# Performance work log

Measured on AMD Instinct MI355X. Metric: run time of the kernel, lower is better.

## Reference

```python
import jax, jax.numpy as jnp
import numpy as np

INPUT_DIM = 1024
OUT_DIM = 1024
ORDER = 4
EXPANSION_POINT = 0.0


def setup_inputs() -> dict:
    key = jax.random.key(0)
    k_x, k_c = jax.random.split(key)
    x = jax.random.normal(k_x, (8192, INPUT_DIM), dtype=jnp.float32)
    coeffs = jax.random.normal(k_c, (OUT_DIM, INPUT_DIM, ORDER), dtype=jnp.float32) * 0.01
    bias = jnp.zeros((1, OUT_DIM), dtype=jnp.float32)
    return {"x": x, "coeffs": coeffs, "bias": bias}


def reference(x, coeffs, bias):
    # x: [..., input_dim] -> flatten leading dims
    outshape = x.shape[:-1] + (OUT_DIM,)
    xf = x.reshape(-1, INPUT_DIM)
    x_shifted = xf - EXPANSION_POINT
    # powers P[n, i, k] = x_shifted^k, k = 0..order-1 (0**0 == 1, matching torch)
    powers = jnp.power(x_shifted[:, :, None], jnp.arange(ORDER, dtype=x.dtype))
    # y[n, o] = sum_{i,k} P[n,i,k] * coeffs[o,i,k]  -- single GEMM-like contraction
    y = jnp.einsum('nik,oik->no', powers, coeffs)
    y = y + bias
    return y.reshape(outshape)
```

## Files before the change

kernel.cpp:

```cpp
#include <hip/hip_runtime.h>
#include <stdint.h>

#define IN_DIM 1024
#define OUT_DIM 1024
#define NROWS 8192
#define KD 3072

#define BM 256
#define BN 128
#define BK 64
#define NT (KD / BK)

typedef __bf16 bf16x8 __attribute__((ext_vector_type(8)));
typedef float f32x4 __attribute__((ext_vector_type(4)));
typedef unsigned short us8 __attribute__((ext_vector_type(8)));
typedef unsigned int u32;

#define AS1 __attribute__((address_space(1)))
#define AS3 __attribute__((address_space(3)))

__device__ __forceinline__ unsigned short f2bf(float f) {
    u32 u = __builtin_bit_cast(u32, f);
    u32 r = (u + 0x7fffu + ((u >> 16) & 1u)) >> 16;
    return (unsigned short)r;
}

__global__ __launch_bounds__(256) void prep_coeffs(const float* __restrict__ c,
                                                   const float* __restrict__ bias,
                                                   unsigned short* __restrict__ B,
                                                   float* __restrict__ bias2) {
    const int o = blockIdx.x;
    const float4* row = reinterpret_cast<const float4*>(c + (size_t)o * (IN_DIM * 4));
    unsigned short* Bo = B + (size_t)o * KD;
    float s = 0.f;
    for (int i = threadIdx.x; i < IN_DIM; i += 256) {
        float4 v = row[i];
        s += v.x;
        Bo[i]        = f2bf(v.y);
        Bo[1024 + i] = f2bf(v.z);
        Bo[2048 + i] = f2bf(v.w);
    }
#pragma unroll
    for (int off = 32; off; off >>= 1) s += __shfl_down(s, off);
    __shared__ float red[4];
    if ((threadIdx.x & 63) == 0) red[threadIdx.x >> 6] = s;
    __syncthreads();
    if (threadIdx.x == 0) bias2[o] = bias[o] + red[0] + red[1] + red[2] + red[3];
}

__global__ __launch_bounds__(256) void prep_powers(const float* __restrict__ x,
                                                   unsigned short* __restrict__ A) {
    int t = blockIdx.x * blockDim.x + threadIdx.x;
    int n = t >> 8;
    int i4 = (t & 255) * 4;
    float4 v = reinterpret_cast<const float4*>(x)[t];
    unsigned short* An = A + (size_t)n * KD + i4;
    float xs[4] = {v.x, v.y, v.z, v.w};
    unsigned short b1[4], b2[4], b3[4];
#pragma unroll
    for (int j = 0; j < 4; ++j) {
        float x1 = xs[j], x2 = x1 * x1, x3 = x2 * x1;
        b1[j] = f2bf(x1); b2[j] = f2bf(x2); b3[j] = f2bf(x3);
    }
    ushort4 p1 = {b1[0], b1[1], b1[2], b1[3]};
    ushort4 p2 = {b2[0], b2[1], b2[2], b2[3]};
    ushort4 p3 = {b3[0], b3[1], b3[2], b3[3]};
    *reinterpret_cast<ushort4*>(An)        = p1;
    *reinterpret_cast<ushort4*>(An + 1024) = p2;
    *reinterpret_cast<ushort4*>(An + 2048) = p3;
}

__global__ __launch_bounds__(512, 1) void taylor_gemm(
    const unsigned short* __restrict__ A,
    const unsigned short* __restrict__ B,
    const float* __restrict__ bias2,
    float* __restrict__ C) {
    __shared__ alignas(16) unsigned short sA[3][BM * BK];
    __shared__ alignas(16) unsigned short sB[3][BN * BK];

    const int tid = threadIdx.x;
    const int lane = tid & 63;
    const int wid = tid >> 6;
    const int wr = wid >> 1;
    const int wc = wid & 1;
    const int gx = blockIdx.x, gy = blockIdx.y;

    const char* Ab = (const char*)A;
    const char* Bb = (const char*)B;
    const int cs = ((lane & 7) ^ (lane >> 3)) * 8;
    size_t aSrc[4], bSrc[2];
    int aDst[4], bDst[2];
#pragma unroll
    for (int u = 0; u < 4; ++u) {
        int row = gx * BM + u * 64 + wid * 8 + (lane >> 3);
        aSrc[u] = ((size_t)row * KD + cs) * 2;
        aDst[u] = (u * 64 + wid * 8) * BK;
    }
#pragma unroll
    for (int u = 0; u < 2; ++u) {
        int row = gy * BN + u * 64 + wid * 8 + (lane >> 3);
        bSrc[u] = ((size_t)row * KD + cs) * 2;
        bDst[u] = (u * 64 + wid * 8) * BK;
    }

    auto stage_unit = [&](int b, int kt, int u) {
        size_t koff = (size_t)kt * (BK * 2);
        if (u < 4)
            __builtin_amdgcn_global_load_lds(
                (const AS1 void*)(Ab + aSrc[u] + koff),
                (AS3 void*)(&sA[b][aDst[u]]), 16, 0, 0);
        else
            __builtin_amdgcn_global_load_lds(
                (const AS1 void*)(Bb + bSrc[u - 4] + koff),
                (AS3 void*)(&sB[b][bDst[u - 4]]), 16, 0, 0);
    };

    int aSw[2], bSw[2];
#pragma unroll
    for (int ks = 0; ks < 2; ++ks) {
        int sw = ((ks * 4 + (lane >> 4)) ^ (lane & 7)) * 8;
        aSw[ks] = (wr * 64 + (lane & 15)) * BK + sw;
        bSw[ks] = (wc * 64 + (lane & 15)) * BK + sw;
    }

    f32x4 acc[4][4] = {};

#pragma unroll
    for (int u = 0; u < 6; ++u) stage_unit(0, 0, u);
#pragma unroll
    for (int u = 0; u < 6; ++u) stage_unit(1, 1, u);

    for (int kt = 0; kt < NT; ++kt) {
        const int cb = kt % 3;
        const int nb = (kt + 2) % 3;
        if (kt < NT - 1) asm volatile("s_waitcnt vmcnt(6)" ::: "memory");
        else             asm volatile("s_waitcnt vmcnt(0)" ::: "memory");
        __builtin_amdgcn_s_barrier();
        __builtin_amdgcn_sched_barrier(0);

        const unsigned short* sAc = &sA[cb][0];
        const unsigned short* sBc = &sB[cb][0];
        const bool doStage = (kt < NT - 2);

        bf16x8 bfr[4][2];
#pragma unroll
        for (int n = 0; n < 4; ++n)
#pragma unroll
            for (int ks = 0; ks < 2; ++ks)
                bfr[n][ks] = __builtin_bit_cast(bf16x8,
                    *reinterpret_cast<const us8*>(&sBc[bSw[ks] + n * 16 * BK]));

#pragma unroll
        for (int m = 0; m < 4; ++m) {
            bf16x8 af[2];
#pragma unroll
            for (int ks = 0; ks < 2; ++ks)
                af[ks] = __builtin_bit_cast(bf16x8,
                    *reinterpret_cast<const us8*>(&sAc[aSw[ks] + m * 16 * BK]));
            if (doStage) {
                stage_unit(nb, kt + 2, m);
                if (m < 2) stage_unit(nb, kt + 2, 4 + m);
            }
            asm volatile("s_waitcnt lgkmcnt(0)" ::: "memory");
            __builtin_amdgcn_sched_barrier(0);
            __builtin_amdgcn_s_setprio(1);
#pragma unroll
            for (int n = 0; n < 4; ++n)
#pragma unroll
                for (int ks = 0; ks < 2; ++ks)
                    acc[m][n] = __builtin_amdgcn_mfma_f32_16x16x32_bf16(
                        af[ks], bfr[n][ks], acc[m][n], 0, 0, 0);
            __builtin_amdgcn_s_setprio(0);
        }
    }

    const int colBase = gy * BN + wc * 64 + (lane & 15);
    const int rowBase = gx * BM + wr * 64 + (lane >> 4) * 4;
#pragma unroll
    for (int n = 0; n < 4; ++n) {
        int col = colBase + n * 16;
        float bv = bias2[col];
#pragma unroll
        for (int m = 0; m < 4; ++m) {
            int row = rowBase + m * 16;
#pragma unroll
            for (int r = 0; r < 4; ++r)
                C[(size_t)(row + r) * OUT_DIM + col] = acc[m][n][r] + bv;
        }
    }
}

__global__ void taylor_naive(const float* __restrict__ x, const float* __restrict__ coeffs,
                             const float* __restrict__ bias, float* __restrict__ out) {
    int n = blockIdx.x;
    __shared__ float P[IN_DIM * 4];
    for (int i = threadIdx.x; i < IN_DIM; i += blockDim.x) {
        float xv = x[(size_t)n * IN_DIM + i];
        P[i * 4 + 0] = 1.f;
        P[i * 4 + 1] = xv;
        P[i * 4 + 2] = xv * xv;
        P[i * 4 + 3] = xv * xv * xv;
    }
    __syncthreads();
    for (int o = threadIdx.x; o < OUT_DIM; o += blockDim.x) {
        float s = bias[o];
        const float* c = coeffs + (size_t)o * (IN_DIM * 4);
        for (int i = 0; i < IN_DIM; ++i) {
            float4 cv = *reinterpret_cast<const float4*>(c + i * 4);
            s += cv.x * P[i * 4 + 0] + cv.y * P[i * 4 + 1] +
                 cv.z * P[i * 4 + 2] + cv.w * P[i * 4 + 3];
        }
        out[(size_t)n * OUT_DIM + o] = s;
    }
}

extern "C" void kernel_launch(void* const* d_in, const int* in_sizes, int n_in,
                              void* d_out, int out_size, void* d_ws, size_t ws_size,
                              hipStream_t stream) {
    const float* x = (const float*)d_in[0];
    const float* coeffs = (const float*)d_in[1];
    const float* bias = (const float*)d_in[2];
    float* out = (float*)d_out;

    const size_t needA = (size_t)NROWS * KD * 2;
    const size_t needB = (size_t)OUT_DIM * KD * 2;
    const size_t needBias = OUT_DIM * sizeof(float);

    if (ws_size >= needA + needB + needBias) {
        unsigned short* A = (unsigned short*)d_ws;
        unsigned short* B = (unsigned short*)((char*)d_ws + needA);
        float* bias2 = (float*)((char*)d_ws + needA + needB);
        prep_coeffs<<<OUT_DIM, 256, 0, stream>>>(coeffs, bias, B, bias2);
        prep_powers<<<(NROWS * IN_DIM / 4) / 256, 256, 0, stream>>>(x, A);
        dim3 grid(NROWS / BM, OUT_DIM / BN);
        taylor_gemm<<<grid, 512, 0, stream>>>(A, B, bias2, out);
    } else {
        taylor_naive<<<NROWS, 256, 0, stream>>>(x, coeffs, bias, out);
    }
}
```

Measured before the change: 90.06 us.

## Double-buffer LDS fragments in registers and overlap reads with MFMA

Restructures the GEMM main loop so the next k-tile's LDS fragments are loaded into a second register set while the current tile's 32 MFMAs run, unrolled by two to ping-pong register buffers. Global-to-LDS staging is now issued all at once per iteration, with a full vmcnt(0) wait. Launch bounds are raised to two blocks per CU. Together these aim to hide LDS latency and raise occupancy, at the cost of roughly doubled fragment registers, which could spill under the tighter register budget. The full vmcnt wait may also expose global load latency, and the LDS footprint may not actually allow two blocks per CU.

```diff
diff --git a/kernel.cpp b/kernel.cpp
--- a/kernel.cpp
+++ b/kernel.cpp
@@ -23,6 +23,10 @@
     u32 u = __builtin_bit_cast(u32, f);
     u32 r = (u + 0x7fffu + ((u >> 16) & 1u)) >> 16;
     return (unsigned short)r;
+}
+
+__device__ __forceinline__ bf16x8 ld8(const unsigned short* p) {
+    return __builtin_bit_cast(bf16x8, *reinterpret_cast<const us8*>(p));
 }
 
 __global__ __launch_bounds__(256) void prep_coeffs(const float* __restrict__ c,
@@ -70,7 +74,7 @@
     *reinterpret_cast<ushort4*>(An + 2048) = p3;
 }
 
-__global__ __launch_bounds__(512, 1) void taylor_gemm(
+__global__ __launch_bounds__(512, 2) void taylor_gemm(
     const unsigned short* __restrict__ A,
     const unsigned short* __restrict__ B,
     const float* __restrict__ bias2,
@@ -103,16 +107,18 @@
         bDst[u] = (u * 64 + wid * 8) * BK;
     }
 
-    auto stage_unit = [&](int b, int kt, int u) {
+    auto stage_all = [&](int b, int kt) {
         size_t koff = (size_t)kt * (BK * 2);
-        if (u < 4)
+#pragma unroll
+        for (int u = 0; u < 4; ++u)
             __builtin_amdgcn_global_load_lds(
                 (const AS1 void*)(Ab + aSrc[u] + koff),
                 (AS3 void*)(&sA[b][aDst[u]]), 16, 0, 0);
-        else
+#pragma unroll
+        for (int u = 0; u < 2; ++u)
             __builtin_amdgcn_global_load_lds(
-                (const AS1 void*)(Bb + bSrc[u - 4] + koff),
-                (AS3 void*)(&sB[b][bDst[u - 4]]), 16, 0, 0);
+                (const AS1 void*)(Bb + bSrc[u] + koff),
+                (AS3 void*)(&sB[b][bDst[u]]), 16, 0, 0);
     };
 
     int aSw[2], bSw[2];
@@ -123,56 +129,60 @@
         bSw[ks] = (wc * 64 + (lane & 15)) * BK + sw;
     }
 
+    bf16x8 fa0[4][2], fb0[4][2], fa1[4][2], fb1[4][2];
     f32x4 acc[4][4] = {};
 
-#pragma unroll
-    for (int u = 0; u < 6; ++u) stage_unit(0, 0, u);
-#pragma unroll
-    for (int u = 0; u < 6; ++u) stage_unit(1, 1, u);
-
-    for (int kt = 0; kt < NT; ++kt) {
-        const int cb = kt % 3;
-        const int nb = (kt + 2) % 3;
-        if (kt < NT - 1) asm volatile("s_waitcnt vmcnt(6)" ::: "memory");
-        else             asm volatile("s_waitcnt vmcnt(0)" ::: "memory");
-        __builtin_amdgcn_s_barrier();
-        __builtin_amdgcn_sched_barrier(0);
-
-        const unsigned short* sAc = &sA[cb][0];
-        const unsigned short* sBc = &sB[cb][0];
-        const bool doStage = (kt < NT - 2);
-
-        bf16x8 bfr[4][2];
+    auto read_frags = [&](bf16x8 (&fa)[4][2], bf16x8 (&fb)[4][2], int b) {
+        const unsigned short* sAc = &sA[b][0];
+        const unsigned short* sBc = &sB[b][0];
 #pragma unroll
         for (int n = 0; n < 4; ++n)
 #pragma unroll
             for (int ks = 0; ks < 2; ++ks)
-                bfr[n][ks] = __builtin_bit_cast(bf16x8,
-                    *reinterpret_cast<const us8*>(&sBc[bSw[ks] + n * 16 * BK]));
-
-#pragma unroll
-        for (int m = 0; m < 4; ++m) {
-            bf16x8 af[2];
+                fb[n][ks] = ld8(&sBc[bSw[ks] + n * 16 * BK]);
+#pragma unroll
+        for (int m = 0; m < 4; ++m)
 #pragma unroll
             for (int ks = 0; ks < 2; ++ks)
-                af[ks] = __builtin_bit_cast(bf16x8,
-                    *reinterpret_cast<const us8*>(&sAc[aSw[ks] + m * 16 * BK]));
-            if (doStage) {
-                stage_unit(nb, kt + 2, m);
-                if (m < 2) stage_unit(nb, kt + 2, 4 + m);
-            }
-            asm volatile("s_waitcnt lgkmcnt(0)" ::: "memory");
-            __builtin_amdgcn_sched_barrier(0);
-            __builtin_amdgcn_s_setprio(1);
+                fa[m][ks] = ld8(&sAc[aSw[ks] + m * 16 * BK]);
+    };
+
+    auto mfma_all = [&](bf16x8 (&fa)[4][2], bf16x8 (&fb)[4][2]) {
+        __builtin_amdgcn_s_setprio(1);
+#pragma unroll
+        for (int m = 0; m < 4; ++m)
 #pragma unroll
             for (int n = 0; n < 4; ++n)
 #pragma unroll
                 for (int ks = 0; ks < 2; ++ks)
                     acc[m][n] = __builtin_amdgcn_mfma_f32_16x16x32_bf16(
-                        af[ks], bfr[n][ks], acc[m][n], 0, 0, 0);
-            __builtin_amdgcn_s_setprio(0);
-        }
-    }
+                        fa[m][ks], fb[n][ks], acc[m][n], 0, 0, 0);
+        __builtin_amdgcn_s_setprio(0);
+    };
+
+    stage_all(0, 0);
+    stage_all(1, 1);
+    asm volatile("s_waitcnt vmcnt(6)" ::: "memory");
+    __builtin_amdgcn_s_barrier();
+    __builtin_amdgcn_sched_barrier(0);
+    read_frags(fa0, fb0, 0);
+
+#define TAYLOR_ITER(kt, FAc, FBc, FAn, FBn)                                   \
+    {                                                                         \
+        asm volatile("s_waitcnt vmcnt(0)" ::: "memory");                      \
+        __builtin_amdgcn_s_barrier();                                         \
+        __builtin_amdgcn_sched_barrier(0);                                    \
+        if ((kt) < NT - 2) stage_all(((kt) + 2) % 3, (kt) + 2);               \
+        if ((kt) < NT - 1) read_frags(FAn, FBn, ((kt) + 1) % 3);              \
+        __builtin_amdgcn_sched_barrier(0);                                    \
+        mfma_all(FAc, FBc);                                                   \
+    }
+
+    for (int kt = 0; kt < NT; kt += 2) {
+        TAYLOR_ITER(kt,     fa0, fb0, fa1, fb1);
+        TAYLOR_ITER(kt + 1, fa1, fb1, fa0, fb0);
+    }
+#undef TAYLOR_ITER
 
     const int colBase = gy * BN + wc * 64 + (lane & 15);
     const int rowBase = gx * BM + wr * 64 + (lane >> 4) * 4;
```

Measured after the change: 87.91 us. 1.02x faster.

## Software-pipeline LDS fragment loads with register double buffering across K tiles

Applied to the files above, without the earlier changes.

Restructures the GEMM main loop so each K tile's MFMAs are split into two halves. The next tile's B and first-half A fragments are read from LDS into a second register buffer while the second half of the current tile computes. Global-to-LDS staging is spread into two groups of three units with a vmcnt(3) wait. The goal is to hide LDS read latency and the per-tile lgkmcnt stalls behind MFMA work. In exchange it raises register pressure and adds an extra barrier per tile.

```diff
diff --git a/kernel.cpp b/kernel.cpp
--- a/kernel.cpp
+++ b/kernel.cpp
@@ -23,6 +23,10 @@
     u32 u = __builtin_bit_cast(u32, f);
     u32 r = (u + 0x7fffu + ((u >> 16) & 1u)) >> 16;
     return (unsigned short)r;
+}
+
+__device__ __forceinline__ bf16x8 ld8(const unsigned short* p) {
+    return __builtin_bit_cast(bf16x8, *reinterpret_cast<const us8*>(p));
 }
 
 __global__ __launch_bounds__(256) void prep_coeffs(const float* __restrict__ c,
@@ -123,56 +127,99 @@
         bSw[ks] = (wc * 64 + (lane & 15)) * BK + sw;
     }
 
+    bf16x8 bA[4][2], bB[4][2];
+    bf16x8 aA[2][2], aB[2][2];
     f32x4 acc[4][4] = {};
 
 #pragma unroll
     for (int u = 0; u < 6; ++u) stage_unit(0, 0, u);
 #pragma unroll
     for (int u = 0; u < 6; ++u) stage_unit(1, 1, u);
-
-    for (int kt = 0; kt < NT; ++kt) {
-        const int cb = kt % 3;
-        const int nb = (kt + 2) % 3;
-        if (kt < NT - 1) asm volatile("s_waitcnt vmcnt(6)" ::: "memory");
-        else             asm volatile("s_waitcnt vmcnt(0)" ::: "memory");
-        __builtin_amdgcn_s_barrier();
-        __builtin_amdgcn_sched_barrier(0);
-
-        const unsigned short* sAc = &sA[cb][0];
-        const unsigned short* sBc = &sB[cb][0];
-        const bool doStage = (kt < NT - 2);
-
-        bf16x8 bfr[4][2];
-#pragma unroll
-        for (int n = 0; n < 4; ++n)
-#pragma unroll
-            for (int ks = 0; ks < 2; ++ks)
-                bfr[n][ks] = __builtin_bit_cast(bf16x8,
-                    *reinterpret_cast<const us8*>(&sBc[bSw[ks] + n * 16 * BK]));
-
-#pragma unroll
-        for (int m = 0; m < 4; ++m) {
-            bf16x8 af[2];
-#pragma unroll
-            for (int ks = 0; ks < 2; ++ks)
-                af[ks] = __builtin_bit_cast(bf16x8,
-                    *reinterpret_cast<const us8*>(&sAc[aSw[ks] + m * 16 * BK]));
-            if (doStage) {
-                stage_unit(nb, kt + 2, m);
-                if (m < 2) stage_unit(nb, kt + 2, 4 + m);
-            }
-            asm volatile("s_waitcnt lgkmcnt(0)" ::: "memory");
-            __builtin_amdgcn_sched_barrier(0);
-            __builtin_amdgcn_s_setprio(1);
-#pragma unroll
-            for (int n = 0; n < 4; ++n)
-#pragma unroll
-                for (int ks = 0; ks < 2; ++ks)
-                    acc[m][n] = __builtin_amdgcn_mfma_f32_16x16x32_bf16(
-                        af[ks], bfr[n][ks], acc[m][n], 0, 0, 0);
-            __builtin_amdgcn_s_setprio(0);
-        }
-    }
+    asm volatile("s_waitcnt vmcnt(6)" ::: "memory");
+    __builtin_amdgcn_s_barrier();
+    __builtin_amdgcn_sched_barrier(0);
+#pragma unroll
+    for (int n = 0; n < 4; ++n)
+#pragma unroll
+        for (int ks = 0; ks < 2; ++ks)
+            bA[n][ks] = ld8(&sB[0][bSw[ks] + n * 16 * BK]);
+#pragma unroll
+    for (int mi = 0; mi < 2; ++mi)
+#pragma unroll
+        for (int ks = 0; ks < 2; ++ks)
+            aA[mi][ks] = ld8(&sA[0][aSw[ks] + mi * 16 * BK]);
+
+#define TAYLOR_TILE(kt, CURB, CURA, NXTB, NXTA)                               \
+    {                                                                         \
+                              \
+        bf16x8 a23[2][2];                                                     \
+        _Pragma("unroll")                                                     \
+        for (int mi = 0; mi < 2; ++mi)                                        \
+            _Pragma("unroll")                                                 \
+            for (int ks = 0; ks < 2; ++ks)                                    \
+                a23[mi][ks] = ld8(&sA[(kt) % 3][aSw[ks] + (2 + mi) * 16 * BK]); \
+        if ((kt) + 2 < NT) {                                                  \
+            stage_unit(((kt) + 2) % 3, (kt) + 2, 0);                          \
+            stage_unit(((kt) + 2) % 3, (kt) + 2, 4);                          \
+            stage_unit(((kt) + 2) % 3, (kt) + 2, 1);                          \
+        }                                                                     \
+        __builtin_amdgcn_sched_barrier(0);                                    \
+         \
+        __builtin_amdgcn_s_setprio(1);                                        \
+        _Pragma("unroll")                                                     \
+        for (int mi = 0; mi < 2; ++mi)                                        \
+            _Pragma("unroll")                                                 \
+            for (int n = 0; n < 4; ++n)                                       \
+                _Pragma("unroll")                                             \
+                for (int ks = 0; ks < 2; ++ks)                                \
+                    acc[mi][n] = __builtin_amdgcn_mfma_f32_16x16x32_bf16(     \
+                        CURA[mi][ks], CURB[n][ks], acc[mi][n], 0, 0, 0);      \
+        __builtin_amdgcn_s_setprio(0);                                        \
+        __builtin_amdgcn_sched_barrier(0);                                    \
+                    \
+        if ((kt) + 2 < NT) asm volatile("s_waitcnt vmcnt(3)" ::: "memory");   \
+        else               asm volatile("s_waitcnt vmcnt(0)" ::: "memory");   \
+        __builtin_amdgcn_s_barrier();                                         \
+        __builtin_amdgcn_sched_barrier(0);                                    \
+                     \
+        if ((kt) + 1 < NT) {                                                  \
+            _Pragma("unroll")                                                 \
+            for (int n = 0; n < 4; ++n)                                       \
+                _Pragma("unroll")                                             \
+                for (int ks = 0; ks < 2; ++ks)                                \
+                    NXTB[n][ks] = ld8(&sB[((kt) + 1) % 3][bSw[ks] + n * 16 * BK]); \
+            _Pragma("unroll")                                                 \
+            for (int mi = 0; mi < 2; ++mi)                                    \
+                _Pragma("unroll")                                             \
+                for (int ks = 0; ks < 2; ++ks)                                \
+                    NXTA[mi][ks] = ld8(&sA[((kt) + 1) % 3][aSw[ks] + mi * 16 * BK]); \
+        }                                                                     \
+        if ((kt) + 2 < NT) {                                                  \
+            stage_unit(((kt) + 2) % 3, (kt) + 2, 5);                          \
+            stage_unit(((kt) + 2) % 3, (kt) + 2, 2);                          \
+            stage_unit(((kt) + 2) % 3, (kt) + 2, 3);                          \
+        }                                                                     \
+        __builtin_amdgcn_sched_barrier(0);                                    \
+                    \
+        __builtin_amdgcn_s_setprio(1);                                        \
+        _Pragma("unroll")                                                     \
+        for (int mi = 0; mi < 2; ++mi)                                        \
+            _Pragma("unroll")                                                 \
+            for (int n = 0; n < 4; ++n)                                       \
+                _Pragma("unroll")                                             \
+                for (int ks = 0; ks < 2; ++ks)                                \
+                    acc[2 + mi][n] = __builtin_amdgcn_mfma_f32_16x16x32_bf16( \
+                        a23[mi][ks], CURB[n][ks], acc[2 + mi][n], 0, 0, 0);   \
+        __builtin_amdgcn_s_setprio(0);                                        \
+        __builtin_amdgcn_s_barrier();   \
+        __builtin_amdgcn_sched_barrier(0);                                    \
+    }
+
+    for (int kt = 0; kt < NT; kt += 2) {
+        TAYLOR_TILE(kt,     bA, aA, bB, aB);
+        TAYLOR_TILE(kt + 1, bB, aB, bA, aA);
+    }
+#undef TAYLOR_TILE
 
     const int colBase = gy * BN + wc * 64 + (lane & 15);
     const int rowBase = gx * BM + wr * 64 + (lane >> 4) * 4;
```

Measured after the change: 75.84 us. 1.19x faster.
